# Kernel optimization log

Measured on AMD Instinct MI355X. Metric: run time of the kernel, lower is better.

Reference implementation:

```python
import jax, jax.numpy as jnp
import numpy as np

B, S, D_IN = 4, 2048, 512
H, D_OUT = 8, 64


def setup_inputs() -> dict:
    key = jax.random.key(0)
    k1, k2, k3 = jax.random.split(key, 3)
    x = jax.random.normal(k1, (B, S, D_IN), dtype=jnp.float32)
    # matches torch init: w ~ U(-0.8, 0.8), wo ~ U(-1, 1)
    w = jax.random.uniform(k2, (H, 3, D_IN, D_OUT), dtype=jnp.float32, minval=-0.8, maxval=0.8)
    wo = jax.random.uniform(k3, (H * D_OUT, D_OUT), dtype=jnp.float32, minval=-1.0, maxval=1.0)
    return {"x": x, "w": w, "wo": wo}


def reference(x, w, wo):
    d_out = w.shape[-1]
    # batched per-head projections: [B, H, S, D_OUT]
    q = jnp.einsum('bsi,hio->bhso', x, w[:, 0])
    k = jnp.einsum('bsi,hio->bhso', x, w[:, 1])
    v = jnp.einsum('bsi,hio->bhso', x, w[:, 2])
    scores = jnp.einsum('bhso,bhto->bhst', q, k) / jnp.sqrt(jnp.asarray(d_out, x.dtype))
    attn = jax.nn.softmax(scores, axis=-1)
    o = jnp.einsum('bhst,bhto->bhso', attn, v)  # [B, H, S, D_OUT]
    # concat heads along feature dim (head order matches torch cat order)
    o = jnp.transpose(o, (0, 2, 1, 3)).reshape(x.shape[0], x.shape[1], -1)
    return jnp.matmul(o, wo)
```

## Files before the change

kernel.cpp:

```cpp
#include <hip/hip_runtime.h>
#include <cstdint>
#include <cstddef>

#define S_LEN 2048
#define DIN   512
#define DOUT  64
#define NB    4
#define NH    8

typedef __attribute__((ext_vector_type(8))) short bf16x8;
typedef __attribute__((ext_vector_type(8))) _Float16 f16x8;
typedef __attribute__((ext_vector_type(4))) float f32x4;
typedef __attribute__((ext_vector_type(16))) float f32x16;

static __device__ __forceinline__ f32x4 mfma16(bf16x8 a, bf16x8 b, f32x4 c) {
    return __builtin_amdgcn_mfma_f32_16x16x32_bf16(a, b, c, 0, 0, 0);
}
static __device__ __forceinline__ f32x16 mfma32h(f16x8 a, f16x8 b, f32x16 c) {
    return __builtin_amdgcn_mfma_f32_32x32x16_f16(a, b, c, 0, 0, 0);
}

static __device__ __forceinline__ uint16_t f2bf(float x) {
    uint32_t u = __builtin_bit_cast(uint32_t, x);
    u += 0x7fffu + ((u >> 16) & 1u);
    return (uint16_t)(u >> 16);
}
static __device__ __forceinline__ float bf2f(uint16_t h) {
    uint32_t u = ((uint32_t)h) << 16;
    return __builtin_bit_cast(float, u);
}
static __device__ __forceinline__ uint32_t cvt_pk_bf16(float lo, float hi) {
    uint32_t r;
    asm("v_cvt_pk_bf16_f32 %0, %1, %2" : "=v"(r) : "v"(lo), "v"(hi));
    return r;
}
static __device__ __forceinline__ uint32_t cvt_pkrtz_f16(float lo, float hi) {
    return __builtin_bit_cast(uint32_t, __builtin_amdgcn_cvt_pkrtz(lo, hi));
}

__global__ __launch_bounds__(256) void prep_w(
    const float* __restrict__ w, const float* __restrict__ wo,
    uint16_t* __restrict__ whiT, uint16_t* __restrict__ wloT,
    uint16_t* __restrict__ woT)
{
    __shared__ float tile[64][65];
    const int blk = blockIdx.x;
    const int t = threadIdx.x;
    const int tq = t >> 6, tr = t & 63;

    if (blk < 192) {
        const int hp = blk >> 3, i0 = (blk & 7) * 64;
        const int p = hp % 3;
        const float s = (p == 0) ? 0.18033688011112042f : 1.0f;
        const float* __restrict__ src = w + (size_t)hp * (DIN * DOUT);
        #pragma unroll
        for (int r = 0; r < 16; ++r) {
            const int ir = r * 4 + tq;
            tile[ir][tr] = src[(size_t)(i0 + ir) * DOUT + tr];
        }
        __syncthreads();
        uint16_t* __restrict__ dh = whiT + (size_t)hp * (DOUT * DIN);
        uint16_t* __restrict__ dl = wloT + (size_t)hp * (DOUT * DIN);
        #pragma unroll
        for (int r = 0; r < 16; ++r) {
            const int o = r * 4 + tq;
            const float v = tile[tr][o] * s;
            const uint16_t hi = f2bf(v);
            dh[(size_t)o * DIN + i0 + tr] = hi;
            dl[(size_t)o * DIN + i0 + tr] = f2bf(v - bf2f(hi));
        }
    } else {
        const int i0 = (blk - 192) * 64;
        #pragma unroll
        for (int r = 0; r < 16; ++r) {
            const int ir = r * 4 + tq;
            tile[ir][tr] = wo[(size_t)(i0 + ir) * DOUT + tr];
        }
        __syncthreads();
        #pragma unroll
        for (int r = 0; r < 16; ++r) {
            const int o = r * 4 + tq;
            woT[(size_t)o * DIN + i0 + tr] = f2bf(tile[tr][o]);
        }
    }
}

__global__ __launch_bounds__(256) void split_x(
    const float* __restrict__ x, uint16_t* __restrict__ xhi, uint16_t* __restrict__ xlo)
{
    const size_t idx = ((size_t)blockIdx.x * 256 + threadIdx.x) * 8;
    const float4 a = *(const float4*)(x + idx);
    const float4 b = *(const float4*)(x + idx + 4);
    const float xv[8] = {a.x, a.y, a.z, a.w, b.x, b.y, b.z, b.w};
    union { uint16_t u[8]; uint4 v; } H, L;
    #pragma unroll
    for (int j = 0; j < 8; ++j) {
        const uint16_t hi = f2bf(xv[j]);
        H.u[j] = hi;
        L.u[j] = f2bf(xv[j] - bf2f(hi));
    }
    *(uint4*)(xhi + idx) = H.v;
    *(uint4*)(xlo + idx) = L.v;
}

__global__ __launch_bounds__(256, 2) void gemm_qkv(
    const uint16_t* __restrict__ xhi, const uint16_t* __restrict__ xlo,
    const uint16_t* __restrict__ whiT, const uint16_t* __restrict__ wloT,
    uint16_t* __restrict__ qf, uint16_t* __restrict__ kfm,
    uint16_t* __restrict__ vfm)
{
    __shared__ __align__(16) uint16_t lds[4 * 128 * 64];

    const int bid = blockIdx.x;
    const int xcd = bid & 7, wi = bid >> 3;
    const int mt = xcd * 8 + wi / 12, nt = wi % 12;
    const int m0 = mt * 128, n0 = nt * 128;
    const int tid = threadIdx.x;
    const int l = tid & 63, w = tid >> 6;
    const int g = l >> 4, lm = l & 15;
    const int wm = w >> 1, wn = w & 1;

    const f32x4 Z = {0.f, 0.f, 0.f, 0.f};
    f32x4 acc[4][4];
    #pragma unroll
    for (int a = 0; a < 4; ++a)
        #pragma unroll
        for (int b = 0; b < 4; ++b) acc[a][b] = Z;

    int srow[4], scol[4];
    #pragma unroll
    for (int i = 0; i < 4; ++i) {
        const int c = i * 256 + tid;
        srow[i] = c >> 3;
        scol[i] = ((c & 7) * 8) ^ ((srow[i] & 7) << 3);
    }

    for (int kt = 0; kt < 8; ++kt) {
        const int k0 = kt * 64;
        uint4 stg[16];
        #pragma unroll
        for (int i = 0; i < 4; ++i) {
            const size_t aoff = (size_t)(m0 + srow[i]) * DIN + k0 + scol[i];
            const size_t boff = (size_t)(n0 + srow[i]) * DIN + k0 + scol[i];
            stg[i * 4 + 0] = *(const uint4*)(xhi  + aoff);
            stg[i * 4 + 1] = *(const uint4*)(xlo  + aoff);
            stg[i * 4 + 2] = *(const uint4*)(whiT + boff);
            stg[i * 4 + 3] = *(const uint4*)(wloT + boff);
        }
        #pragma unroll
        for (int i = 0; i < 4; ++i) {
            const int c8 = (i * 256 + tid) * 8;
            *(uint4*)&lds[c8]                 = stg[i * 4 + 0];
            *(uint4*)&lds[128 * 64 + c8]      = stg[i * 4 + 1];
            *(uint4*)&lds[2 * 128 * 64 + c8]  = stg[i * 4 + 2];
            *(uint4*)&lds[3 * 128 * 64 + c8]  = stg[i * 4 + 3];
        }
        __syncthreads();

        bf16x8 ah[4][2], al[4][2];
        #pragma unroll
        for (int mi = 0; mi < 4; ++mi) {
            const int r = wm * 64 + mi * 16 + lm;
            const int rb = r * 128;
            #pragma unroll
            for (int kk = 0; kk < 2; ++kk) {
                const int cb = (kk * 64 + g * 16) ^ ((r & 7) << 4);
                ah[mi][kk] = *(const bf16x8*)((const char*)lds + rb + cb);
                al[mi][kk] = *(const bf16x8*)((const char*)lds + 16384 + rb + cb);
            }
        }
        #pragma unroll
        for (int ni = 0; ni < 4; ++ni) {
            const int r = wn * 64 + ni * 16 + lm;
            const int rb = r * 128;
            bf16x8 bh[2], bl[2];
            #pragma unroll
            for (int kk = 0; kk < 2; ++kk) {
                const int cb = (kk * 64 + g * 16) ^ ((r & 7) << 4);
                bh[kk] = *(const bf16x8*)((const char*)lds + 32768 + rb + cb);
                bl[kk] = *(const bf16x8*)((const char*)lds + 49152 + rb + cb);
            }
            #pragma unroll
            for (int mi = 0; mi < 4; ++mi) {
                acc[mi][ni] = mfma16(ah[mi][0], bh[0], acc[mi][ni]);
                acc[mi][ni] = mfma16(ah[mi][1], bh[1], acc[mi][ni]);
                acc[mi][ni] = mfma16(ah[mi][0], bl[0], acc[mi][ni]);
                acc[mi][ni] = mfma16(ah[mi][1], bl[1], acc[mi][ni]);
                acc[mi][ni] = mfma16(al[mi][0], bh[0], acc[mi][ni]);
                acc[mi][ni] = mfma16(al[mi][1], bh[1], acc[mi][ni]);
            }
        }
        __syncthreads();
    }

    #pragma unroll
    for (int ni = 0; ni < 4; ++ni) {
        const int n = n0 + wn * 64 + ni * 16 + lm;
        const int hp = n >> 6, o = n & 63;
        const int h = hp / 3, p = hp - h * 3;
        if (p == 0) {
            #pragma unroll
            for (int mi = 0; mi < 4; ++mi) {
                #pragma unroll
                for (int j = 0; j < 4; ++j) {
                    const int m = m0 + wm * 64 + mi * 16 + 4 * g + j;
                    const int b = m >> 11, s = m & 2047;
                    const size_t idx = ((size_t)(b * NH + h) * S_LEN + s) * DOUT + o;
                    const _Float16 hv = (_Float16)acc[mi][ni][j];
                    qf[idx] = __builtin_bit_cast(uint16_t, hv);
                }
            }
        } else if (p == 1) {
            #pragma unroll
            for (int mi = 0; mi < 4; ++mi) {
                const int m = m0 + wm * 64 + mi * 16 + 4 * g;
                const int b = m >> 11, s = m & 2047;
                const int tile = s >> 6, sr = s & 63;
                const int gam = ((sr >> 5) * 4 + (o >> 4)) * 64 + ((o >> 3) & 1) * 32 + (sr & 31);
                uint16_t* __restrict__ dst =
                    kfm + ((size_t)((b * NH + h) * 32 + tile)) * 4096 + gam * 8 + (o & 7);
                #pragma unroll
                for (int j = 0; j < 4; ++j) {
                    const _Float16 hv = (_Float16)acc[mi][ni][j];
                    dst[j * 8] = __builtin_bit_cast(uint16_t, hv);
                }
            }
        } else {
            #pragma unroll
            for (int mi = 0; mi < 4; ++mi) {
                const int m = m0 + wm * 64 + mi * 16 + 4 * g;
                const int b = m >> 11, s = m & 2047;
                const int tile = s >> 6, sc = s & 63;
                const int gam = ((o >> 5) * 4 + (sc >> 4)) * 64 + ((sc >> 3) & 1) * 32 + (o & 31);
                union { _Float16 h[4]; uint2 u; } pk;
                pk.h[0] = (_Float16)acc[mi][ni][0];
                pk.h[1] = (_Float16)acc[mi][ni][1];
                pk.h[2] = (_Float16)acc[mi][ni][2];
                pk.h[3] = (_Float16)acc[mi][ni][3];
                *(uint2*)(vfm + ((size_t)((b * NH + h) * 32 + tile)) * 4096
                              + gam * 8 + (sc & 7)) = pk.u;
            }
        }
    }
}

__global__ __launch_bounds__(256, 2) void attn_fwd(
    const uint16_t* __restrict__ qf, const uint16_t* __restrict__ kfm,
    const uint16_t* __restrict__ vfm, uint16_t* __restrict__ oc)
{
    __shared__ __align__(16) char smem[32768];
    char* __restrict__ vbufs = smem + 16384;

    const int bid = blockIdx.x;
    const int qt = (bid >> 3) & 15, bh = (bid & 7) + 8 * (bid >> 7);
    const int tid = threadIdx.x;
    const int l = tid & 63, wq = tid >> 6;
    const int L = l >> 5, lq = l & 31;
    const size_t base = (size_t)bh * (S_LEN * DOUT);

    const uint16_t* __restrict__ ktb = kfm + (size_t)bh * 131072;
    const uint16_t* __restrict__ vtb = vfm + (size_t)bh * 131072;
    const uint32_t t16 = (uint32_t)tid * 16;

    const int qrow = qt * 128 + wq * 32 + lq;
    const uint16_t* qp = qf + base + (size_t)qrow * DOUT;
    f16x8 qv[4];
    #pragma unroll
    for (int dsub = 0; dsub < 4; ++dsub)
        qv[dsub] = *(const f16x8*)(qp + dsub * 16 + L * 8);

    f32x16 Zv;
    #pragma unroll
    for (int r = 0; r < 16; ++r) Zv[r] = 0.f;
    f32x16 Oa[2] = {Zv, Zv};
    float m_run = -INFINITY, l_run = 0.f;

    uint4 kA0, kA1, vA0, vA1, kB0, kB1, vB0, vB1;

    auto qk_step = [&](const char* kb2, f32x16* dst) {
        __builtin_amdgcn_s_setprio(1);
        #pragma unroll
        for (int ks = 0; ks < 2; ++ks) {
            f32x16 s = Zv;
            #pragma unroll
            for (int dsub = 0; dsub < 4; ++dsub) {
                const uint32_t off = (uint32_t)(((ks * 4 + dsub) << 10) + (l << 4));
                const f16x8 kfr = *(const f16x8*)(kb2 + off);
                s = mfma32h(kfr, qv[dsub], s);
            }
            dst[ks] = s;
        }
        __builtin_amdgcn_s_setprio(0);
    };

    kA0 = *(const uint4*)(ktb + (size_t)tid * 8);
    kA1 = *(const uint4*)(ktb + 2048 + (size_t)tid * 8);
    vA0 = *(const uint4*)(vtb + (size_t)tid * 8);
    vA1 = *(const uint4*)(vtb + 2048 + (size_t)tid * 8);
    kB0 = *(const uint4*)(ktb + 4096 + (size_t)tid * 8);
    kB1 = *(const uint4*)(ktb + 6144 + (size_t)tid * 8);
    vB0 = *(const uint4*)(vtb + 4096 + (size_t)tid * 8);
    vB1 = *(const uint4*)(vtb + 6144 + (size_t)tid * 8);
    *(uint4*)(smem + t16)          = kA0;
    *(uint4*)(smem + 4096 + t16)   = kA1;
    *(uint4*)(vbufs + t16)         = vA0;
    *(uint4*)(vbufs + 4096 + t16)  = vA1;
    *(uint4*)(smem + 8192 + t16)   = kB0;
    *(uint4*)(smem + 12288 + t16)  = kB1;
    *(uint4*)(vbufs + 8192 + t16)  = vB0;
    *(uint4*)(vbufs + 12288 + t16) = vB1;
    {
        const size_t o2 = (size_t)2 * 4096 + tid * 8, o3 = (size_t)3 * 4096 + tid * 8;
        kA0 = *(const uint4*)(ktb + o2); kA1 = *(const uint4*)(ktb + o2 + 2048);
        vA0 = *(const uint4*)(vtb + o2); vA1 = *(const uint4*)(vtb + o2 + 2048);
        kB0 = *(const uint4*)(ktb + o3); kB1 = *(const uint4*)(ktb + o3 + 2048);
        vB0 = *(const uint4*)(vtb + o3); vB1 = *(const uint4*)(vtb + o3 + 2048);
    }
    asm volatile("s_waitcnt lgkmcnt(0)" ::: "memory");
    __builtin_amdgcn_s_barrier();
    __builtin_amdgcn_sched_barrier(0);

    f32x16 saA[2], saB[2];
    qk_step(smem, saA);

    auto iter = [&](int kt, f32x16* sa, f32x16* sb,
                    uint4& k0, uint4& k1, uint4& v0, uint4& v1) {
        qk_step(smem + ((kt + 1) & 1) * 8192, sb);
        const char* __restrict__ vb = vbufs + (kt & 1) * 8192;
        const uint32_t vo = (uint32_t)(l << 4);
        const f16x8 pv0 = *(const f16x8*)(vb + (0u << 10) + vo);
        const f16x8 pv1 = *(const f16x8*)(vb + (1u << 10) + vo);
        const f16x8 pv2 = *(const f16x8*)(vb + (2u << 10) + vo);
        const f16x8 pv3 = *(const f16x8*)(vb + (3u << 10) + vo);
        const f16x8 pv4 = *(const f16x8*)(vb + (4u << 10) + vo);
        const f16x8 pv5 = *(const f16x8*)(vb + (5u << 10) + vo);
        const f16x8 pv6 = *(const f16x8*)(vb + (6u << 10) + vo);
        const f16x8 pv7 = *(const f16x8*)(vb + (7u << 10) + vo);
        __builtin_amdgcn_sched_barrier(0);

        float mx[16];
        #pragma unroll
        for (int r = 0; r < 16; ++r) mx[r] = fmaxf(sa[0][r], sa[1][r]);
        #pragma unroll
        for (int st = 8; st >= 1; st >>= 1)
            #pragma unroll
            for (int r = 0; r < st; ++r) mx[r] = fmaxf(mx[r], mx[r + st]);
        float pmax = mx[0];
        pmax = fmaxf(pmax, __shfl_xor(pmax, 32));

        if (!__all(pmax - m_run <= 8.f)) {
            const float m_new = fmaxf(m_run, pmax);
            const float alpha = __builtin_amdgcn_exp2f(m_run - m_new);
            m_run = m_new;
            #pragma unroll
            for (int r = 0; r < 16; ++r) { Oa[0][r] *= alpha; Oa[1][r] *= alpha; }
            l_run *= alpha;
        }

        #pragma unroll
        for (int ks = 0; ks < 2; ++ks)
            #pragma unroll
            for (int r = 0; r < 16; ++r)
                sa[ks][r] = __builtin_amdgcn_exp2f(sa[ks][r] - m_run);

        float sm[16];
        #pragma unroll
        for (int r = 0; r < 16; ++r) sm[r] = sa[0][r] + sa[1][r];
        #pragma unroll
        for (int st = 8; st >= 1; st >>= 1)
            #pragma unroll
            for (int r = 0; r < st; ++r) sm[r] += sm[r + st];
        float lsum = sm[0];
        lsum += __shfl_xor(lsum, 32);
        l_run += lsum;

        f16x8 pfrag[4];
        #pragma unroll
        for (int ks = 0; ks < 2; ++ks) {
            uint32_t a0 = cvt_pkrtz_f16(sa[ks][0], sa[ks][1]);
            uint32_t a1 = cvt_pkrtz_f16(sa[ks][2], sa[ks][3]);
            uint32_t a2 = cvt_pkrtz_f16(sa[ks][4], sa[ks][5]);
            uint32_t a3 = cvt_pkrtz_f16(sa[ks][6], sa[ks][7]);
            asm volatile("v_permlane32_swap_b32 %0, %1" : "+v"(a0), "+v"(a2));
            asm volatile("v_permlane32_swap_b32 %0, %1" : "+v"(a1), "+v"(a3));
            union { uint32_t w[4]; f16x8 v; } u;
            u.w[0] = a0; u.w[1] = a1; u.w[2] = a2; u.w[3] = a3;
            pfrag[2 * ks] = u.v;
            uint32_t b0 = cvt_pkrtz_f16(sa[ks][8],  sa[ks][9]);
            uint32_t b1 = cvt_pkrtz_f16(sa[ks][10], sa[ks][11]);
            uint32_t b2 = cvt_pkrtz_f16(sa[ks][12], sa[ks][13]);
            uint32_t b3 = cvt_pkrtz_f16(sa[ks][14], sa[ks][15]);
            asm volatile("v_permlane32_swap_b32 %0, %1" : "+v"(b0), "+v"(b2));
            asm volatile("v_permlane32_swap_b32 %0, %1" : "+v"(b1), "+v"(b3));
            union { uint32_t w[4]; f16x8 v; } u2;
            u2.w[0] = b0; u2.w[1] = b1; u2.w[2] = b2; u2.w[3] = b3;
            pfrag[2 * ks + 1] = u2.v;
        }

        __builtin_amdgcn_s_setprio(1);
        Oa[0] = mfma32h(pv0, pfrag[0], Oa[0]);
        Oa[0] = mfma32h(pv1, pfrag[1], Oa[0]);
        Oa[0] = mfma32h(pv2, pfrag[2], Oa[0]);
        Oa[0] = mfma32h(pv3, pfrag[3], Oa[0]);
        Oa[1] = mfma32h(pv4, pfrag[0], Oa[1]);
        Oa[1] = mfma32h(pv5, pfrag[1], Oa[1]);
        Oa[1] = mfma32h(pv6, pfrag[2], Oa[1]);
        Oa[1] = mfma32h(pv7, pfrag[3], Oa[1]);
        __builtin_amdgcn_s_setprio(0);

        __builtin_amdgcn_s_barrier();
        {
            char* __restrict__ kb = smem + (kt & 1) * 8192;
            char* __restrict__ vbw = vbufs + (kt & 1) * 8192;
            *(uint4*)(kb + t16)         = k0;
            *(uint4*)(kb + 4096 + t16)  = k1;
            *(uint4*)(vbw + t16)        = v0;
            *(uint4*)(vbw + 4096 + t16) = v1;
            const int tk = (kt + 4 < 32) ? kt + 4 : 0;
            const size_t toff = (size_t)tk * 4096 + tid * 8;
            k0 = *(const uint4*)(ktb + toff);
            k1 = *(const uint4*)(ktb + toff + 2048);
            v0 = *(const uint4*)(vtb + toff);
            v1 = *(const uint4*)(vtb + toff + 2048);
        }
        asm volatile("s_waitcnt lgkmcnt(0)" ::: "memory");
        __builtin_amdgcn_sched_barrier(0);
        __builtin_amdgcn_s_barrier();
    };

    for (int t = 0; t < 16; ++t) {
        iter(2 * t,     saA, saB, kA0, kA1, vA0, vA1);
        iter(2 * t + 1, saB, saA, kB0, kB1, vB0, vB1);
    }

    const int b = bh >> 3, hh = bh & 7;
    const float li = 1.f / l_run;
    const int srow = qt * 128 + wq * 32 + lq;
    const size_t rbase = ((size_t)b * S_LEN + srow) * (NH * DOUT) + hh * DOUT;
    #pragma unroll
    for (int dh = 0; dh < 2; ++dh) {
        #pragma unroll
        for (int rq = 0; rq < 4; ++rq) {
            const int d0 = dh * 32 + rq * 8 + L * 4;
            uint2 val;
            val.x = cvt_pk_bf16(Oa[dh][rq * 4 + 0] * li, Oa[dh][rq * 4 + 1] * li);
            val.y = cvt_pk_bf16(Oa[dh][rq * 4 + 2] * li, Oa[dh][rq * 4 + 3] * li);
            *(uint2*)(oc + rbase + d0) = val;
        }
    }
}

__global__ __launch_bounds__(256) void oproj(
    const uint16_t* __restrict__ oc, const uint16_t* __restrict__ woT,
    float* __restrict__ out)
{
    const int mt = blockIdx.x;
    const int tid = threadIdx.x;
    const int l = tid & 63, w = tid >> 6;
    const int g = l >> 4, lm = l & 15;
    const int m0 = mt * 64 + w * 16;
    const f32x4 Z = {0.f, 0.f, 0.f, 0.f};
    f32x4 acc[4] = {Z, Z, Z, Z};
    const uint16_t* __restrict__ arow = oc + (size_t)(m0 + lm) * (NH * DOUT);
    for (int kc = 0; kc < 16; ++kc) {
        const bf16x8 a = *(const bf16x8*)(arow + kc * 32 + g * 8);
        #pragma unroll
        for (int nt = 0; nt < 4; ++nt) {
            const bf16x8 bfr = *(const bf16x8*)(woT + (size_t)(nt * 16 + lm) * (NH * DOUT) + kc * 32 + g * 8);
            acc[nt] = mfma16(a, bfr, acc[nt]);
        }
    }
    #pragma unroll
    for (int nt = 0; nt < 4; ++nt)
        #pragma unroll
        for (int j = 0; j < 4; ++j)
            out[(size_t)(m0 + 4 * g + j) * DOUT + nt * 16 + lm] = acc[nt][j];
}

extern "C" void kernel_launch(void* const* d_in, const int* in_sizes, int n_in,
                              void* d_out, int out_size, void* d_ws, size_t ws_size,
                              hipStream_t stream) {
    const float* x  = (const float*)d_in[0];
    const float* w  = (const float*)d_in[1];
    const float* wo = (const float*)d_in[2];
    float* out = (float*)d_out;

    char* ws = (char*)d_ws;
    uint16_t* qf   = (uint16_t*)(ws);
    uint16_t* kfm  = (uint16_t*)(ws + 8388608);
    uint16_t* vfm  = (uint16_t*)(ws + 16777216);
    uint16_t* xhi  = (uint16_t*)(ws + 25165824);
    uint16_t* xlo  = (uint16_t*)(ws + 33554432);
    uint16_t* whiT = (uint16_t*)(ws + 41943040);
    uint16_t* wloT = (uint16_t*)(ws + 43515904);
    uint16_t* woT  = (uint16_t*)(ws + 45088768);
    uint16_t* oc   = xhi;

    hipLaunchKernelGGL(prep_w, dim3(200), dim3(256), 0, stream, w, wo, whiT, wloT, woT);
    hipLaunchKernelGGL(split_x, dim3(2048), dim3(256), 0, stream, x, xhi, xlo);
    hipLaunchKernelGGL(gemm_qkv, dim3(768), dim3(256), 0, stream,
                       xhi, xlo, whiT, wloT, qf, kfm, vfm);
    hipLaunchKernelGGL(attn_fwd, dim3(512), dim3(256), 0, stream,
                       qf, kfm, vfm, oc);
    hipLaunchKernelGGL(oproj, dim3(128), dim3(256), 0, stream, oc, woT, out);
}
```

Measured before the change: 116.3 us.

## Split attention KV range in two and merge partial outputs

Splits each attention block's key/value sequence into two halves, launching twice as many blocks. Each writes an unnormalized-then-normalized fp16 partial output plus its running max and sum. A new merge kernel rescales the two partials with the log-sum-exp weights and writes the bf16 concatenated output. The aim is more parallelism and better CU occupancy on the 512-block grid, at the cost of an extra kernel launch and extra global traffic for the partials.

```diff
diff --git a/kernel.cpp b/kernel.cpp
--- a/kernel.cpp
+++ b/kernel.cpp
@@ -246,20 +246,22 @@
 
 __global__ __launch_bounds__(256, 2) void attn_fwd(
     const uint16_t* __restrict__ qf, const uint16_t* __restrict__ kfm,
-    const uint16_t* __restrict__ vfm, uint16_t* __restrict__ oc)
+    const uint16_t* __restrict__ vfm,
+    uint16_t* __restrict__ part0, uint16_t* __restrict__ part1,
+    float2* __restrict__ ml)
 {
     __shared__ __align__(16) char smem[32768];
     char* __restrict__ vbufs = smem + 16384;
 
     const int bid = blockIdx.x;
-    const int qt = (bid >> 3) & 15, bh = (bid & 7) + 8 * (bid >> 7);
+    const int half = bid >> 9, qt = (bid >> 5) & 15, bh = bid & 31;
     const int tid = threadIdx.x;
     const int l = tid & 63, wq = tid >> 6;
     const int L = l >> 5, lq = l & 31;
     const size_t base = (size_t)bh * (S_LEN * DOUT);
 
-    const uint16_t* __restrict__ ktb = kfm + (size_t)bh * 131072;
-    const uint16_t* __restrict__ vtb = vfm + (size_t)bh * 131072;
+    const uint16_t* __restrict__ ktb = kfm + (size_t)bh * 131072 + (size_t)half * 65536;
+    const uint16_t* __restrict__ vtb = vfm + (size_t)bh * 131072 + (size_t)half * 65536;
     const uint32_t t16 = (uint32_t)tid * 16;
 
     const int qrow = qt * 128 + wq * 32 + lq;
@@ -416,7 +418,7 @@
             *(uint4*)(kb + 4096 + t16)  = k1;
             *(uint4*)(vbw + t16)        = v0;
             *(uint4*)(vbw + 4096 + t16) = v1;
-            const int tk = (kt + 4 < 32) ? kt + 4 : 0;
+            const int tk = (kt + 4 < 16) ? kt + 4 : 0;
             const size_t toff = (size_t)tk * 4096 + tid * 8;
             k0 = *(const uint4*)(ktb + toff);
             k1 = *(const uint4*)(ktb + toff + 2048);
@@ -428,26 +430,61 @@
         __builtin_amdgcn_s_barrier();
     };
 
-    for (int t = 0; t < 16; ++t) {
+    for (int t = 0; t < 8; ++t) {
         iter(2 * t,     saA, saB, kA0, kA1, vA0, vA1);
         iter(2 * t + 1, saB, saA, kB0, kB1, vB0, vB1);
     }
 
-    const int b = bh >> 3, hh = bh & 7;
+    uint16_t* __restrict__ pd = half ? part1 : part0;
     const float li = 1.f / l_run;
     const int srow = qt * 128 + wq * 32 + lq;
-    const size_t rbase = ((size_t)b * S_LEN + srow) * (NH * DOUT) + hh * DOUT;
+    const size_t rbase = ((size_t)bh * S_LEN + srow) * DOUT;
     #pragma unroll
     for (int dh = 0; dh < 2; ++dh) {
         #pragma unroll
         for (int rq = 0; rq < 4; ++rq) {
             const int d0 = dh * 32 + rq * 8 + L * 4;
             uint2 val;
-            val.x = cvt_pk_bf16(Oa[dh][rq * 4 + 0] * li, Oa[dh][rq * 4 + 1] * li);
-            val.y = cvt_pk_bf16(Oa[dh][rq * 4 + 2] * li, Oa[dh][rq * 4 + 3] * li);
-            *(uint2*)(oc + rbase + d0) = val;
-        }
-    }
+            val.x = cvt_pkrtz_f16(Oa[dh][rq * 4 + 0] * li, Oa[dh][rq * 4 + 1] * li);
+            val.y = cvt_pkrtz_f16(Oa[dh][rq * 4 + 2] * li, Oa[dh][rq * 4 + 3] * li);
+            *(uint2*)(pd + rbase + d0) = val;
+        }
+    }
+    if (L == 0) {
+        float2 v; v.x = m_run; v.y = l_run;
+        ml[((size_t)half << 16) | ((size_t)bh << 11) | (size_t)srow] = v;
+    }
+}
+
+__global__ __launch_bounds__(256) void merge_o(
+    const uint16_t* __restrict__ part0, const uint16_t* __restrict__ part1,
+    const float2* __restrict__ ml, uint16_t* __restrict__ oc)
+{
+    const int g = blockIdx.x * 256 + threadIdx.x;
+    const int row = g >> 3, dp = (g & 7) * 8;
+    const int bh = row >> 11, s = row & 2047;
+
+    const float2 ml0 = ml[row];
+    const float2 ml1 = ml[65536 + row];
+    const float m = fmaxf(ml0.x, ml1.x);
+    float w0 = ml0.y * __builtin_amdgcn_exp2f(ml0.x - m);
+    float w1 = ml1.y * __builtin_amdgcn_exp2f(ml1.x - m);
+    const float inv = 1.f / (w0 + w1);
+    w0 *= inv; w1 *= inv;
+
+    const size_t poff = (size_t)row * 64 + dp;
+    union { uint4 u; f16x8 v; } a, b;
+    a.u = *(const uint4*)(part0 + poff);
+    b.u = *(const uint4*)(part1 + poff);
+    union { uint32_t w[4]; uint4 u; } r;
+    #pragma unroll
+    for (int j = 0; j < 4; ++j) {
+        const float o0 = w0 * (float)a.v[2 * j]     + w1 * (float)b.v[2 * j];
+        const float o1 = w0 * (float)a.v[2 * j + 1] + w1 * (float)b.v[2 * j + 1];
+        r.w[j] = cvt_pk_bf16(o0, o1);
+    }
+    const int bb = bh >> 3, h = bh & 7;
+    *(uint4*)(oc + ((size_t)(bb * S_LEN + s) * (NH * DOUT)) + h * DOUT + dp) = r.u;
 }
 
 __global__ __launch_bounds__(256) void oproj(
@@ -486,21 +523,26 @@
     float* out = (float*)d_out;
 
     char* ws = (char*)d_ws;
-    uint16_t* qf   = (uint16_t*)(ws);
-    uint16_t* kfm  = (uint16_t*)(ws + 8388608);
-    uint16_t* vfm  = (uint16_t*)(ws + 16777216);
-    uint16_t* xhi  = (uint16_t*)(ws + 25165824);
-    uint16_t* xlo  = (uint16_t*)(ws + 33554432);
-    uint16_t* whiT = (uint16_t*)(ws + 41943040);
-    uint16_t* wloT = (uint16_t*)(ws + 43515904);
-    uint16_t* woT  = (uint16_t*)(ws + 45088768);
-    uint16_t* oc   = xhi;
+    uint16_t* qf    = (uint16_t*)(ws);
+    uint16_t* kfm   = (uint16_t*)(ws + 8388608);
+    uint16_t* vfm   = (uint16_t*)(ws + 16777216);
+    uint16_t* xhi   = (uint16_t*)(ws + 25165824);
+    uint16_t* xlo   = (uint16_t*)(ws + 33554432);
+    uint16_t* part1 = (uint16_t*)(ws + 41943040);
+    float2*   ml    = (float2*)  (ws + 50331648);
+    uint16_t* whiT  = (uint16_t*)(ws + 51380224);
+    uint16_t* wloT  = (uint16_t*)(ws + 52953088);
+    uint16_t* woT   = (uint16_t*)(ws + 54525952);
+    uint16_t* oc    = xhi;
+    uint16_t* part0 = xlo;
 
     hipLaunchKernelGGL(prep_w, dim3(200), dim3(256), 0, stream, w, wo, whiT, wloT, woT);
     hipLaunchKernelGGL(split_x, dim3(2048), dim3(256), 0, stream, x, xhi, xlo);
     hipLaunchKernelGGL(gemm_qkv, dim3(768), dim3(256), 0, stream,
                        xhi, xlo, whiT, wloT, qf, kfm, vfm);
-    hipLaunchKernelGGL(attn_fwd, dim3(512), dim3(256), 0, stream,
-                       qf, kfm, vfm, oc);
+    hipLaunchKernelGGL(attn_fwd, dim3(1024), dim3(256), 0, stream,
+                       qf, kfm, vfm, part0, part1, ml);
+    hipLaunchKernelGGL(merge_o, dim3(2048), dim3(256), 0, stream,
+                       part0, part1, ml, oc);
     hipLaunchKernelGGL(oproj, dim3(128), dim3(256), 0, stream, oc, woT, out);
 }
```

After: 123.5 us. 6.2% more time.
